# Optimization experiments

Measured on AMD Instinct MI355X. Metric: run time of the kernel, lower is better.

## Reference

```python
import jax, jax.numpy as jnp
import numpy as np

PAD = 4
KERNEL = 1
MAX_DISP = 4
STRIDE1 = 1
STRIDE2 = 1


def setup_inputs() -> dict:
    key = jax.random.key(0)
    k1, k2 = jax.random.split(key)
    B, C, H, W = 16, 128, 96, 160
    input1 = jax.random.normal(k1, (B, C, H, W), dtype=jnp.float32)
    input2 = jax.random.normal(k2, (B, C, H, W), dtype=jnp.float32)
    return {"input1": input1, "input2": input2}


def _correlation(input1, input2):
    # FlowNet-style patch cross-correlation (corr_multiply=1).
    # Output[b, d, y, x] = sum_{c, patch} I1[b,c,patch(y,x)] * I2[b,c,patch(y+dy,x+dx)] / (K*K*C)
    B, C, H, W = input1.shape
    kr = (KERNEL - 1) // 2  # kernel radius (0 for KERNEL=1)
    p1 = jnp.pad(input1, ((0, 0), (0, 0), (PAD, PAD), (PAD, PAD)))
    p2 = jnp.pad(input2, ((0, 0), (0, 0), (PAD, PAD), (PAD, PAD)))
    norm = jnp.float32(KERNEL * KERNEL * C)
    outs = []
    for dy in range(-MAX_DISP, MAX_DISP + 1, STRIDE2):
        for dx in range(-MAX_DISP, MAX_DISP + 1, STRIDE2):
            acc = jnp.zeros((B, H, W), dtype=input1.dtype)
            for ki in range(-kr, kr + 1):
                for kj in range(-kr, kr + 1):
                    a = p1[:, :, PAD + ki:PAD + ki + H, PAD + kj:PAD + kj + W]
                    b = p2[:, :, PAD + ki + dy:PAD + ki + dy + H,
                              PAD + kj + dx:PAD + kj + dx + W]
                    acc = acc + jnp.sum(a * b, axis=1)
            outs.append(acc / norm)
    return jnp.stack(outs, axis=1)  # [B, (2*md/s2+1)^2, H, W]


def reference(input1, input2):
    return _correlation(input1, input2)
```

## Files before the change

### kernel.cpp

```cpp
#include <hip/hip_runtime.h>
#include <stdint.h>

typedef __bf16 bf16;
typedef __attribute__((ext_vector_type(4))) __bf16 bf16x4;
typedef __attribute__((ext_vector_type(8))) __bf16 bf16x8;
typedef __attribute__((ext_vector_type(4))) float f32x4;
typedef __attribute__((ext_vector_type(4))) unsigned int u32x4;

#define W_ 160
#define H_ 96
#define C_ 128
#define B_ 16
#define HW_ (H_ * W_)
#define NXT 10
#define NYB4 24
#define NBLK (B_ * NYB4 * NXT)
#define SLICEB 10240
#define YB 40960
#define ROWSB 2048
#define CHB (12 * ROWSB)
#define WSSTR 1312

__device__ float g_zero[16];

__device__ __forceinline__ void g2l16(const void* g, void* l) {
    __builtin_amdgcn_global_load_lds(
        (const __attribute__((address_space(1))) void*)g,
        (__attribute__((address_space(3))) void*)l, 16, 0, 0);
}

__global__ __launch_bounds__(256) void t2_kernel(const float* __restrict__ in2,
                                                 char* __restrict__ o) {
    __shared__ __align__(16) char T[40960];
    const int L   = blockIdx.x;
    const int tid = threadIdx.x;
    const float* src = in2 + (size_t)(L / H_) * C_ * HW_ + (size_t)(L % H_) * W_;
    char* dst = o + (size_t)L * YB;
    const float SC = 1.0f / 128.0f;
#pragma unroll
    for (int rd = 0; rd < 5; ++rd) {
        const int s  = rd * 256 + tid;
        const int cq = s / 40;
        const int x4 = s - cq * 40;
        const float* p = src + (size_t)(4 * cq) * HW_ + 4 * x4;
        const float4 v0 = *(const float4*)(p);
        const float4 v1 = *(const float4*)(p + HW_);
        const float4 v2 = *(const float4*)(p + 2 * HW_);
        const float4 v3 = *(const float4*)(p + 3 * HW_);
        const int oq = cq >> 1, half = cq & 1;
#pragma unroll
        for (int xj = 0; xj < 4; ++xj) {
            const int x   = 4 * x4 + xj;
            const int pos = oq ^ ((x >> 2) & 15);
            bf16x4 pk;
            pk[0] = (bf16)(((const float*)&v0)[xj] * SC);
            pk[1] = (bf16)(((const float*)&v1)[xj] * SC);
            pk[2] = (bf16)(((const float*)&v2)[xj] * SC);
            pk[3] = (bf16)(((const float*)&v3)[xj] * SC);
            *(bf16x4*)(T + x * 256 + pos * 16 + half * 8) = pk;
        }
    }
    __syncthreads();
#pragma unroll
    for (int wr = 0; wr < 10; ++wr) {
        const int s2  = wr * 256 + tid;
        const int ck  = s2 / 640;
        const int r   = s2 - ck * 640;
        const int x   = r >> 2;
        const int gsw = r & 3;
        const int gg  = gsw ^ ((x >> 1) & 3);
        const int oo  = ck * 4 + gg;
        const int pos = oo ^ ((x >> 2) & 15);
        const u32x4 v = *(const u32x4*)(T + x * 256 + pos * 16);
        *(u32x4*)(dst + (size_t)s2 * 16) = v;
    }
}

__global__ __launch_bounds__(256, 2) void corr_mfma5(const float* __restrict__ in1,
                                                     const char* __restrict__ in2t,
                                                     float* __restrict__ out) {
    __shared__ __align__(16) char Bsm[3 * CHB];

    const int L   = ((int)blockIdx.x & 7) * (NBLK / 8) + ((int)blockIdx.x >> 3);
    const int b   = L / (NYB4 * NXT);
    const int rem = L % (NYB4 * NXT);
    const int yb  = rem / NXT;
    const int xt  = rem % NXT;
    const int x0  = xt * 16, y0 = yb * 4;

    const int tid  = threadIdx.x;
    const int wv   = __builtin_amdgcn_readfirstlane(tid >> 6);
    const int lane = tid & 63;
    const int n    = lane & 15;
    const int g    = lane >> 4;
    const int y    = y0 + wv;

    const char* i2tb = in2t + (size_t)b * (H_ * YB);

    const char* srow[6];
    bool stgv[6];
#pragma unroll
    for (int rd = 0; rd < 6; ++rd) {
        const int s   = rd * 256 + tid;
        const int row = s >> 7;
        const int sl  = s & 127;
        const int gy  = y0 - 4 + row;
        const int x   = x0 - 4 + (sl >> 2);
        stgv[rd] = (sl < 96) && ((unsigned)gy < (unsigned)H_) && ((unsigned)x < (unsigned)W_);
        const int gy_c = min(max(gy, 0), H_ - 1);
        const int ofs  = max((x0 - 4) * 64 + sl * 16, 0);
        srow[rd] = i2tb + (size_t)gy_c * YB + ofs;
    }

    const float* abase = in1 + (size_t)b * C_ * HW_ + (size_t)y * W_ + (x0 + n);
    float a_raw[32];
#pragma unroll
    for (int i = 0; i < 32; ++i)
        a_raw[i] = abase[(size_t)((i >> 3) * 32 + g * 8 + (i & 7)) * HW_];
    bf16x8 afrag[4];
#pragma unroll
    for (int ck = 0; ck < 4; ++ck)
#pragma unroll
        for (int j = 0; j < 8; ++j)
            afrag[ck][j] = (bf16)a_raw[ck * 8 + j];
    asm volatile("s_waitcnt vmcnt(0)" ::: "memory");
    __builtin_amdgcn_sched_barrier(0);

    int rboff[2];
#pragma unroll
    for (int t = 0; t < 2; ++t) {
        const int xl = n + 16 * t;
        const int sw = g ^ (((xl + 12) >> 1) & 3);
        rboff[t] = (xl * 4 + sw) * 16;
    }

    f32x4 acc[9][2];
#pragma unroll
    for (int dyi = 0; dyi < 9; ++dyi)
#pragma unroll
        for (int t = 0; t < 2; ++t)
            acc[dyi][t] = (f32x4){0.f, 0.f, 0.f, 0.f};

#define STAGE(CK, DST)                                                        \
    {                                                                         \
        _Pragma("unroll")                                                     \
        for (int rd = 0; rd < 6; ++rd)                                        \
            g2l16(stgv[rd] ? (const void*)(srow[rd] + (CK) * SLICEB)          \
                           : (const void*)g_zero,                             \
                  (void*)((DST) + rd * 4096 + tid * 16));                     \
    }
#define WAITB(N)                                                              \
    {                                                                         \
        asm volatile("s_waitcnt vmcnt(" #N ")" ::: "memory");                 \
        __builtin_amdgcn_s_barrier();                                         \
        __builtin_amdgcn_sched_barrier(0);                                    \
    }
#define COMPUTE(CK, BUF)                                                      \
    {                                                                         \
        _Pragma("unroll")                                                     \
        for (int dyi = 0; dyi < 9; ++dyi) {                                   \
            const int rowoff = (wv + dyi) * ROWSB;                            \
            _Pragma("unroll")                                                 \
            for (int t = 0; t < 2; ++t) {                                     \
                const bf16x8 bfrag =                                          \
                    *(const bf16x8*)((BUF) + rowoff + rboff[t]);              \
                acc[dyi][t] = __builtin_amdgcn_mfma_f32_16x16x32_bf16(        \
                    afrag[CK], bfrag, acc[dyi][t], 0, 0, 0);                  \
            }                                                                 \
        }                                                                     \
    }

    STAGE(0, Bsm);
    STAGE(1, Bsm + CHB);
    STAGE(2, Bsm + 2 * CHB);
    WAITB(12);
    COMPUTE(0, Bsm);
    WAITB(6);
    STAGE(3, Bsm);
    COMPUTE(1, Bsm + CHB);
    WAITB(6);
    COMPUTE(2, Bsm + 2 * CHB);
    WAITB(0);
    COMPUTE(3, Bsm);
#undef STAGE
#undef WAITB
#undef COMPUTE

    __syncthreads();

    float* wsw = (float*)Bsm + wv * WSSTR;
#pragma unroll
    for (int dyi = 0; dyi < 9; ++dyi)
#pragma unroll
        for (int t = 0; t < 2; ++t)
#pragma unroll
            for (int rr = 0; rr < 4; ++rr) {
                const int m = 4 * g + rr;
                const int d = n + 16 * t - m;
                if ((unsigned)d <= 8u)
                    wsw[(dyi * 9 + d) * 16 + m] = acc[dyi][t][rr];
            }
    __syncthreads();

    const int mm = lane & 15, rg = lane >> 4;
    const size_t ob = (size_t)(b * 81) * HW_ + (size_t)y * W_ + (x0 + mm);
#pragma unroll
    for (int q4 = 0; q4 < 20; ++q4) {
        const int rho = q4 * 4 + rg;
        out[ob + (size_t)rho * HW_] = wsw[rho * 16 + mm];
    }
    if (rg == 0)
        out[ob + (size_t)80 * HW_] = wsw[80 * 16 + mm];
}

extern "C" void kernel_launch(void* const* d_in, const int* in_sizes, int n_in,
                              void* d_out, int out_size, void* d_ws, size_t ws_size,
                              hipStream_t stream) {
    const float* in1 = (const float*)d_in[0];
    const float* in2 = (const float*)d_in[1];
    float* out = (float*)d_out;
    (void)in_sizes; (void)n_in; (void)out_size; (void)ws_size;
    char* in2t = (char*)d_ws;
    hipLaunchKernelGGL(t2_kernel, dim3(B_ * H_), dim3(256), 0, stream, in2, in2t);
    hipLaunchKernelGGL(corr_mfma5, dim3(NBLK), dim3(256), 0, stream, in1, in2t, out);
}
```

Before: 109.6 us.

## Use 8-row tiles with 512-thread blocks and double-buffered staging

Each block now covers 8 output rows with 8 waves instead of 4 rows with 4 waves. The staged input2 halo (rows y0-4..y0+11) is shared by more rows, which cuts redundant halo loads per output. The shared-memory ring drops from triple to double buffering, with explicit LDS-read barriers before each buffer is reused. Staging slots are packed to 96 per row so no thread-slots are wasted. The cost is a shallower prefetch pipeline and larger blocks, which risks exposing load latency and changing occupancy.

After: 101.0 us. 7.8% less time.

```diff
diff --git a/kernel.cpp b/kernel.cpp
--- a/kernel.cpp
+++ b/kernel.cpp
@@ -13,12 +13,12 @@
 #define B_ 16
 #define HW_ (H_ * W_)
 #define NXT 10
-#define NYB4 24
-#define NBLK (B_ * NYB4 * NXT)
+#define NYB8 12
+#define NBLK (B_ * NYB8 * NXT)
 #define SLICEB 10240
 #define YB 40960
-#define ROWSB 2048
-#define CHB (12 * ROWSB)
+#define ROWSB 1536
+#define CHB (16 * ROWSB)
 #define WSSTR 1312
 
 __device__ float g_zero[16];
@@ -76,17 +76,17 @@
     }
 }
 
-__global__ __launch_bounds__(256, 2) void corr_mfma5(const float* __restrict__ in1,
+__global__ __launch_bounds__(512, 4) void corr_mfma6(const float* __restrict__ in1,
                                                      const char* __restrict__ in2t,
                                                      float* __restrict__ out) {
-    __shared__ __align__(16) char Bsm[3 * CHB];
+    __shared__ __align__(16) char Bsm[2 * CHB + 512];
 
     const int L   = ((int)blockIdx.x & 7) * (NBLK / 8) + ((int)blockIdx.x >> 3);
-    const int b   = L / (NYB4 * NXT);
-    const int rem = L % (NYB4 * NXT);
+    const int b   = L / (NYB8 * NXT);
+    const int rem = L % (NYB8 * NXT);
     const int yb  = rem / NXT;
     const int xt  = rem % NXT;
-    const int x0  = xt * 16, y0 = yb * 4;
+    const int x0  = xt * 16, y0 = yb * 8;
 
     const int tid  = threadIdx.x;
     const int wv   = __builtin_amdgcn_readfirstlane(tid >> 6);
@@ -97,34 +97,35 @@
 
     const char* i2tb = in2t + (size_t)b * (H_ * YB);
 
-    const char* srow[6];
-    bool stgv[6];
-#pragma unroll
-    for (int rd = 0; rd < 6; ++rd) {
-        const int s   = rd * 256 + tid;
-        const int row = s >> 7;
-        const int sl  = s & 127;
-        const int gy  = y0 - 4 + row;
-        const int x   = x0 - 4 + (sl >> 2);
-        stgv[rd] = (sl < 96) && ((unsigned)gy < (unsigned)H_) && ((unsigned)x < (unsigned)W_);
+    const float* abase = in1 + (size_t)b * C_ * HW_ + (size_t)y * W_ + (x0 + n);
+    bf16x8 afrag[4];
+#pragma unroll
+    for (int ck = 0; ck < 4; ++ck) {
+        float ar[8];
+#pragma unroll
+        for (int j = 0; j < 8; ++j)
+            ar[j] = abase[(size_t)(ck * 32 + g * 8 + j) * HW_];
+#pragma unroll
+        for (int j = 0; j < 8; ++j)
+            afrag[ck][j] = (bf16)ar[j];
+    }
+    asm volatile("s_waitcnt vmcnt(0)" ::: "memory");
+    __builtin_amdgcn_sched_barrier(0);
+
+    unsigned soff[3];
+    bool     sv[3];
+#pragma unroll
+    for (int rd = 0; rd < 3; ++rd) {
+        const int slot = rd * 512 + tid;
+        const int row  = slot / 96;
+        const int sl   = slot - row * 96;
+        const int gy   = y0 - 4 + row;
+        const int x    = x0 - 4 + (sl >> 2);
+        sv[rd] = ((unsigned)gy < (unsigned)H_) && ((unsigned)x < (unsigned)W_);
         const int gy_c = min(max(gy, 0), H_ - 1);
         const int ofs  = max((x0 - 4) * 64 + sl * 16, 0);
-        srow[rd] = i2tb + (size_t)gy_c * YB + ofs;
-    }
-
-    const float* abase = in1 + (size_t)b * C_ * HW_ + (size_t)y * W_ + (x0 + n);
-    float a_raw[32];
-#pragma unroll
-    for (int i = 0; i < 32; ++i)
-        a_raw[i] = abase[(size_t)((i >> 3) * 32 + g * 8 + (i & 7)) * HW_];
-    bf16x8 afrag[4];
-#pragma unroll
-    for (int ck = 0; ck < 4; ++ck)
-#pragma unroll
-        for (int j = 0; j < 8; ++j)
-            afrag[ck][j] = (bf16)a_raw[ck * 8 + j];
-    asm volatile("s_waitcnt vmcnt(0)" ::: "memory");
-    __builtin_amdgcn_sched_barrier(0);
+        soff[rd] = (unsigned)(gy_c * YB + ofs);
+    }
 
     int rboff[2];
 #pragma unroll
@@ -143,15 +144,22 @@
 
 #define STAGE(CK, DST)                                                        \
     {                                                                         \
+        const char* bck = i2tb + (CK) * SLICEB;                               \
         _Pragma("unroll")                                                     \
-        for (int rd = 0; rd < 6; ++rd)                                        \
-            g2l16(stgv[rd] ? (const void*)(srow[rd] + (CK) * SLICEB)          \
-                           : (const void*)g_zero,                             \
-                  (void*)((DST) + rd * 4096 + tid * 16));                     \
+        for (int rd = 0; rd < 3; ++rd)                                        \
+            g2l16(sv[rd] ? (const void*)(bck + soff[rd])                      \
+                         : (const void*)g_zero,                               \
+                  (void*)((DST) + (rd * 512 + tid) * 16));                    \
     }
 #define WAITB(N)                                                              \
     {                                                                         \
         asm volatile("s_waitcnt vmcnt(" #N ")" ::: "memory");                 \
+        __builtin_amdgcn_s_barrier();                                         \
+        __builtin_amdgcn_sched_barrier(0);                                    \
+    }
+#define RBAR                                                                  \
+    {                                                                         \
+        asm volatile("s_waitcnt lgkmcnt(0)" ::: "memory");                    \
         __builtin_amdgcn_s_barrier();                                         \
         __builtin_amdgcn_sched_barrier(0);                                    \
     }
@@ -172,18 +180,21 @@
 
     STAGE(0, Bsm);
     STAGE(1, Bsm + CHB);
-    STAGE(2, Bsm + 2 * CHB);
-    WAITB(12);
+    WAITB(3);
     COMPUTE(0, Bsm);
-    WAITB(6);
-    STAGE(3, Bsm);
+    RBAR;
+    STAGE(2, Bsm);
+    WAITB(3);
     COMPUTE(1, Bsm + CHB);
-    WAITB(6);
-    COMPUTE(2, Bsm + 2 * CHB);
+    RBAR;
+    STAGE(3, Bsm + CHB);
+    WAITB(3);
+    COMPUTE(2, Bsm);
     WAITB(0);
-    COMPUTE(3, Bsm);
+    COMPUTE(3, Bsm + CHB);
 #undef STAGE
 #undef WAITB
+#undef RBAR
 #undef COMPUTE
 
     __syncthreads();
@@ -222,5 +233,5 @@
     (void)in_sizes; (void)n_in; (void)out_size; (void)ws_size;
     char* in2t = (char*)d_ws;
     hipLaunchKernelGGL(t2_kernel, dim3(B_ * H_), dim3(256), 0, stream, in2, in2t);
-    hipLaunchKernelGGL(corr_mfma5, dim3(NBLK), dim3(256), 0, stream, in1, in2t, out);
-}
+    hipLaunchKernelGGL(corr_mfma6, dim3(NBLK), dim3(512), 0, stream, in1, in2t, out);
+}
```
